# Kernel tuning notes

Measured on AMD Instinct MI355X. Metric: run time of the kernel, lower is better.

## Reference

```python
import jax, jax.numpy as jnp
import numpy as np

DIM = 1024
NUM_HEADS = 16
HEAD_DIM = DIM // NUM_HEADS
SCALE = 1.0 / np.sqrt(HEAD_DIM)
B, S = 2, 2048


def setup_inputs() -> dict:
    key = jax.random.key(0)
    ks = jax.random.split(key, 10)
    std = 1.0 / np.sqrt(DIM)
    return {
        "x": jax.random.normal(ks[0], (B, S, DIM), dtype=jnp.float32),
        "Wq": jax.random.normal(ks[1], (DIM, DIM), dtype=jnp.float32) * std,
        "bq": jnp.zeros((DIM,), dtype=jnp.float32),
        "Wk": jax.random.normal(ks[2], (DIM, DIM), dtype=jnp.float32) * std,
        "bk": jnp.zeros((DIM,), dtype=jnp.float32),
        "Wv": jax.random.normal(ks[3], (DIM, DIM), dtype=jnp.float32) * std,
        "bv": jnp.zeros((DIM,), dtype=jnp.float32),
        "Wo": jax.random.normal(ks[4], (DIM, DIM), dtype=jnp.float32) * std,
        "bo": jnp.zeros((DIM,), dtype=jnp.float32),
        "mobius_weight": jax.random.normal(ks[5], (1,), dtype=jnp.float32) * 0.01,
    }


def _split_heads(t):
    b, s, _ = t.shape
    return t.reshape(b, s, NUM_HEADS, HEAD_DIM).transpose(0, 2, 1, 3)  # bhsd


def reference(x, Wq, bq, Wk, bk, Wv, bv, Wo, bo, mobius_weight):
    q = _split_heads(x @ Wq.T + bq)
    k = _split_heads(x @ Wk.T + bk)
    v = _split_heads(x @ Wv.T + bv)

    # similarity: plain QK^T
    similarity = jnp.einsum('bhqd,bhkd->bhqk', q, k)
    # mobius cross-term: q_omega . k_pi + q_pi . k_omega
    h = HEAD_DIM // 2
    q_om, q_pi = q[..., :h], q[..., h:]
    k_om, k_pi = k[..., :h], k[..., h:]
    mobius = jnp.einsum('bhqd,bhkd->bhqk', q_om, k_pi) + \
             jnp.einsum('bhqd,bhkd->bhqk', q_pi, k_om)

    incidence = (similarity + mobius_weight[0] * mobius) * SCALE
    attn = jax.nn.softmax(incidence, axis=-1)
    out = jnp.einsum('bhqk,bhkd->bhqd', attn, v)
    out = out.transpose(0, 2, 1, 3).reshape(x.shape[0], x.shape[1], DIM)
    return out @ Wo.T + bo
```

## Files before the change

### kernel.cpp

```cpp
#include <hip/hip_runtime.h>


typedef __attribute__((ext_vector_type(8))) short short8;
typedef __attribute__((ext_vector_type(4))) short s16x4;
typedef __attribute__((ext_vector_type(4))) float f32x4;
typedef __attribute__((ext_vector_type(16))) float f32x16;
typedef __attribute__((ext_vector_type(8))) __bf16 bf16x8;
typedef __attribute__((ext_vector_type(4))) unsigned uint4v;

__device__ __forceinline__ float exp2fa(float x) {
  return __builtin_amdgcn_exp2f(x);
}
__device__ __forceinline__ short f2bf(float f) {
  unsigned u = __builtin_bit_cast(unsigned, f);
  u = u + 0x7fffu + ((u >> 16) & 1u);
  return (short)(u >> 16);
}
__device__ __forceinline__ f32x4 mfma16(bf16x8 a, bf16x8 b, f32x4 c) {
  return __builtin_amdgcn_mfma_f32_16x16x32_bf16(a, b, c, 0, 0, 0);
}
__device__ __forceinline__ f32x16 mfma32(bf16x8 a, bf16x8 b, f32x16 c) {
  return __builtin_amdgcn_mfma_f32_32x32x16_bf16(a, b, c, 0, 0, 0);
}
__device__ __forceinline__ void gload_lds16(const void* g, void* l) {
  __builtin_amdgcn_global_load_lds(
      (const __attribute__((address_space(1))) unsigned int*)g,
      (__attribute__((address_space(3))) unsigned int*)l, 16, 0, 0);
}
__device__ __forceinline__ unsigned pkbf(float a, float b) {
  unsigned r;
  asm("v_cvt_pk_bf16_f32 %0, %1, %2" : "=v"(r) : "v"(a), "v"(b));
  return r;
}
__device__ __forceinline__ void plswap(unsigned& a, unsigned& b) {
  asm volatile("v_permlane32_swap_b32 %0, %1" : "+v"(a), "+v"(b));
}
__device__ __forceinline__ bf16x8 pack8(float x0, float x1, float x2, float x3,
                                        float x4, float x5, float x6, float x7) {
  unsigned a0 = pkbf(x0, x1), a1 = pkbf(x2, x3);
  unsigned a2 = pkbf(x4, x5), a3 = pkbf(x6, x7);
  plswap(a0, a2);
  plswap(a1, a3);
  uint4v u = {a0, a1, a2, a3};
  return __builtin_bit_cast(bf16x8, u);
}

__global__ void cast_all_kernel(const float* x, const float* w0, const float* w1,
                                const float* w2, const float* w3, short* xo,
                                short* o0, short* o1, short* o2, short* o3) {
  const float* in; short* out;
  const int r = blockIdx.y;
  size_t off;
  if (r < 4) { in = x; out = xo; off = (size_t)r * 131072; }
  else {
    switch (r) {
      case 4: in = w0; out = o0; break;
      case 5: in = w1; out = o1; break;
      case 6: in = w2; out = o2; break;
      default: in = w3; out = o3; break;
    }
    off = 0;
  }
  const size_t i = off + blockIdx.x * 256 + threadIdx.x;
  const float4* p = (const float4*)in;
  float4 a = p[2 * i], b = p[2 * i + 1];
  short8 o;
  o[0] = f2bf(a.x); o[1] = f2bf(a.y); o[2] = f2bf(a.z); o[3] = f2bf(a.w);
  o[4] = f2bf(b.x); o[5] = f2bf(b.y); o[6] = f2bf(b.z); o[7] = f2bf(b.w);
  ((short8*)out)[i] = o;
}

constexpr int GK = 1024, GN = 1024;
constexpr float QSCALE = 0.125f * 1.44269504088896340736f;

template <int EP>
__device__ __forceinline__ void gemm_body(char* lds, const short* __restrict__ A,
                                          const short* __restrict__ W,
                                          const float* __restrict__ bias,
                                          void* __restrict__ C,
                                          const float* __restrict__ mwp) {
  const int tid = threadIdx.x;
  const int l = tid & 63, w = tid >> 6;
  const int wr = w >> 2, wc = w & 3;
  const int ncb = (wc >> 1) * 64 + (wc & 1) * 16;
  const int m0 = blockIdx.y * 128, n0 = blockIdx.x * 128;

  f32x4 acc[4][2] = {};

  const int srow = tid >> 3, sc8 = tid & 7, wv = tid >> 6;
  for (int kb = 0; kb < GK / 64; ++kb) {
    const int k0 = kb * 64;
#pragma unroll
    for (int p = 0; p < 2; ++p) {
      const int ra = p * 64 + srow;
      gload_lds16(A + (size_t)(m0 + ra) * GK + k0 + ((sc8 ^ (ra & 7)) * 8),
                  lds + p * 8192 + wv * 1024);
      gload_lds16(W + (size_t)(n0 + ra) * GK + k0 + ((sc8 ^ (ra & 7)) * 8),
                  lds + 16384 + p * 8192 + wv * 1024);
    }
    __syncthreads();
#pragma unroll
    for (int ks = 0; ks < 2; ++ks) {
      bf16x8 af[4], bfr[2];
      const int chunk = ks * 4 + (l >> 4);
#pragma unroll
      for (int mf = 0; mf < 4; ++mf) {
        const int mt = wr * 64 + mf * 16 + (l & 15);
        af[mf] = *(const bf16x8*)(lds + mt * 128 + ((chunk ^ (mt & 7)) * 16));
      }
#pragma unroll
      for (int nf = 0; nf < 2; ++nf) {
        const int nt = ncb + nf * 32 + (l & 15);
        bfr[nf] = *(const bf16x8*)(lds + 16384 + nt * 128 + ((chunk ^ (nt & 7)) * 16));
      }
#pragma unroll
      for (int mf = 0; mf < 4; ++mf)
#pragma unroll
        for (int nf = 0; nf < 2; ++nf)
          acc[mf][nf] = mfma16(af[mf], bfr[nf], acc[mf][nf]);
    }
    __syncthreads();
  }

  const float mwv = (EP == 1) ? mwp[0] : 0.f;
#pragma unroll
  for (int mf = 0; mf < 4; ++mf)
#pragma unroll
    for (int nf = 0; nf < 2; ++nf) {
      const int n = n0 + ncb + nf * 32 + (l & 15);
      const int mb = m0 + wr * 64 + mf * 16 + (l >> 4) * 4;
      if (EP == 1) {
        const float bv = bias[n], bv2 = bias[n ^ 32];
        const int h = n >> 6, c = (n >> 3) & 7, j = n & 7;
#pragma unroll
        for (int r = 0; r < 4; ++r) {
          const int m = mb + r;
          const int b = m >> 11, s = m & 2047;
          const float v =
              acc[mf][nf][r] + bv + mwv * (acc[mf][nf ^ 1][r] + bv2);
          ((short*)C)[(size_t)(b * 16 + h) * 131072 + (s >> 5) * 2048 + c * 256 +
                      (s & 31) * 8 + j] = f2bf(v);
        }
      } else if (EP == 2) {
        const int h = n >> 6, w2 = (n >> 5) & 1, dlo = n & 31;
        s16x4 v;
#pragma unroll
        for (int r = 0; r < 4; ++r) v[r] = f2bf(acc[mf][nf][r] + bias[n]);
        const int b = mb >> 11, s = mb & 2047;
        *(s16x4*)((short*)C + (size_t)(b * 16 + h) * 131072 + (s >> 6) * 4096 +
                  w2 * 2048 + ((s >> 3) & 7) * 256 + dlo * 8 + (s & 7)) = v;
      } else {
        const float bv = bias[n];
#pragma unroll
        for (int r = 0; r < 4; ++r) {
          const int m = mb + r;
          float v = acc[mf][nf][r] + bv;
          if (EP == 0) v *= QSCALE;
          if (EP == 3)
            ((float*)C)[(size_t)m * GN + n] = v;
          else
            ((short*)C)[(size_t)m * GN + n] = f2bf(v);
        }
      }
    }
}

__global__ __launch_bounds__(512, 4) void gemm_qkv_kernel(
    const short* __restrict__ A, const short* Wq, const short* Wk, const short* Wv,
    const float* bq, const float* bk, const float* bv, short* q, short* kf,
    short* vf, const float* mw) {
  __shared__ __align__(16) char lds[32768];
  if (blockIdx.z == 0) gemm_body<0>(lds, A, Wq, bq, q, nullptr);
  else if (blockIdx.z == 1) gemm_body<1>(lds, A, Wk, bk, kf, mw);
  else gemm_body<2>(lds, A, Wv, bv, vf, nullptr);
}

__global__ __launch_bounds__(512, 4) void gemm_out_kernel(const short* __restrict__ A,
                                                          const short* __restrict__ W,
                                                          const float* __restrict__ bias,
                                                          float* __restrict__ C) {
  __shared__ __align__(16) char lds[32768];
  gemm_body<3>(lds, A, W, bias, C, nullptr);
}

__global__ __launch_bounds__(256, 3) void attn_kernel(const short* __restrict__ Q,
                                                      const short* __restrict__ Kf,
                                                      const short* __restrict__ Vf,
                                                      short* __restrict__ O) {
  constexpr int S = 2048;
  constexpr int NT = S / 128;
  __shared__ float mbuf[2][32][64];
  __shared__ float lbuf[64];
  const int tid = threadIdx.x;
  const int l = tid & 63, w = tid >> 6;
  const int lo = l & 31, hi = l >> 5;
  const int wq = w & 1, par = w >> 1;
  const int bid = blockIdx.x;
  const int sub = bid >> 3;
  const int x = sub & 31;
  const int y = (bid & 7) * 4 + (sub >> 5);
  const int b = y >> 4, h = y & 15;
  const int q0 = x * 64 + wq * 32;
  const size_t base = (size_t)b * S * 1024 + h * 64;
  const size_t fbase = (size_t)y * 131072;

  bf16x8 qf[4];
  {
    const short* qp = Q + base + (size_t)(q0 + lo) * 1024 + hi * 8;
#pragma unroll
    for (int ds = 0; ds < 4; ++ds) qf[ds] = *(const bf16x8*)(qp + ds * 16);
  }

  const int voff = hi * 256 + lo * 8;
  const short* kp = Kf + fbase + par * 4096 + voff;
  const short* vp = Vf + fbase + par * 4096 + voff;

  bf16x8 kf[8], vf[8];
#pragma unroll
  for (int ds = 0; ds < 4; ++ds) {
    kf[ds]     = *(const bf16x8*)(kp + ds * 512);
    kf[4 + ds] = *(const bf16x8*)(kp + 2048 + ds * 512);
    vf[ds]     = *(const bf16x8*)(vp + ds * 512);
    vf[4 + ds] = *(const bf16x8*)(vp + 2048 + ds * 512);
  }

  f32x16 o0 = {}, o1 = {};
  float lrow = 0.f;

  f32x16 st0 = {}, st1 = {};
  __builtin_amdgcn_s_setprio(1);
#pragma unroll
  for (int ds = 0; ds < 4; ++ds) {
    st0 = mfma32(kf[ds], qf[ds], st0);
    st1 = mfma32(kf[4 + ds], qf[ds], st1);
  }
  __builtin_amdgcn_s_setprio(0);
  kp += 8192;
#pragma unroll
  for (int ds = 0; ds < 4; ++ds) {
    kf[ds]     = *(const bf16x8*)(kp + ds * 512);
    kf[4 + ds] = *(const bf16x8*)(kp + 2048 + ds * 512);
  }

  for (int i = 0; i < NT - 1; ++i) {
#pragma unroll
    for (int r = 0; r < 16; ++r) st0[r] = exp2fa(st0[r]);
#pragma unroll
    for (int r = 0; r < 16; ++r) st1[r] = exp2fa(st1[r]);
    float ts[8];
#pragma unroll
    for (int r = 0; r < 8; ++r)
      ts[r] = (st0[r] + st0[r + 8]) + (st1[r] + st1[r + 8]);
#pragma unroll
    for (int d = 4; d >= 1; d >>= 1)
#pragma unroll
      for (int r = 0; r < 4; ++r)
        if (r < d) ts[r] += ts[r + d];
    lrow += ts[0];

    bf16x8 pf[4];
    pf[0] = pack8(st0[0], st0[1], st0[2], st0[3], st0[4], st0[5], st0[6], st0[7]);
    pf[1] = pack8(st0[8], st0[9], st0[10], st0[11], st0[12], st0[13], st0[14], st0[15]);
    pf[2] = pack8(st1[0], st1[1], st1[2], st1[3], st1[4], st1[5], st1[6], st1[7]);
    pf[3] = pack8(st1[8], st1[9], st1[10], st1[11], st1[12], st1[13], st1[14], st1[15]);

    __builtin_amdgcn_s_setprio(1);
#pragma unroll
    for (int r = 0; r < 16; ++r) { st0[r] = 0.f; st1[r] = 0.f; }
#pragma unroll
    for (int ds = 0; ds < 4; ++ds) {
      st0 = mfma32(kf[ds], qf[ds], st0);
      st1 = mfma32(kf[4 + ds], qf[ds], st1);
    }
#pragma unroll
    for (int kv = 0; kv < 4; ++kv) {
      o0 = mfma32(vf[kv], pf[kv], o0);
      o1 = mfma32(vf[4 + kv], pf[kv], o1);
    }
    __builtin_amdgcn_s_setprio(0);

    kp += 8192;
    vp += 8192;
#pragma unroll
    for (int ds = 0; ds < 4; ++ds) {
      kf[ds]     = *(const bf16x8*)(kp + ds * 512);
      kf[4 + ds] = *(const bf16x8*)(kp + 2048 + ds * 512);
      vf[ds]     = *(const bf16x8*)(vp + ds * 512);
      vf[4 + ds] = *(const bf16x8*)(vp + 2048 + ds * 512);
    }
  }

  {
#pragma unroll
    for (int r = 0; r < 16; ++r) st0[r] = exp2fa(st0[r]);
#pragma unroll
    for (int r = 0; r < 16; ++r) st1[r] = exp2fa(st1[r]);
    float ts[8];
#pragma unroll
    for (int r = 0; r < 8; ++r)
      ts[r] = (st0[r] + st0[r + 8]) + (st1[r] + st1[r + 8]);
#pragma unroll
    for (int d = 4; d >= 1; d >>= 1)
#pragma unroll
      for (int r = 0; r < 4; ++r)
        if (r < d) ts[r] += ts[r + d];
    lrow += ts[0];

    bf16x8 pf[4];
    pf[0] = pack8(st0[0], st0[1], st0[2], st0[3], st0[4], st0[5], st0[6], st0[7]);
    pf[1] = pack8(st0[8], st0[9], st0[10], st0[11], st0[12], st0[13], st0[14], st0[15]);
    pf[2] = pack8(st1[0], st1[1], st1[2], st1[3], st1[4], st1[5], st1[6], st1[7]);
    pf[3] = pack8(st1[8], st1[9], st1[10], st1[11], st1[12], st1[13], st1[14], st1[15]);
    __builtin_amdgcn_s_setprio(1);
#pragma unroll
    for (int kv = 0; kv < 4; ++kv) {
      o0 = mfma32(vf[kv], pf[kv], o0);
      o1 = mfma32(vf[4 + kv], pf[kv], o1);
    }
    __builtin_amdgcn_s_setprio(0);
  }

  lrow += __shfl_xor(lrow, 32);

  if (par == 1) {
#pragma unroll
    for (int g = 0; g < 4; ++g) {
      const int c0 = (2 * g + hi) ^ (lo & 15);
      const int c1 = (8 + 2 * g + hi) ^ (lo & 15);
      f32x4 v0, v1;
#pragma unroll
      for (int r = 0; r < 4; ++r) { v0[r] = o0[g * 4 + r]; v1[r] = o1[g * 4 + r]; }
      *(f32x4*)(&mbuf[wq][lo][c0 * 4]) = v0;
      *(f32x4*)(&mbuf[wq][lo][c1 * 4]) = v1;
    }
    if (hi == 0) lbuf[wq * 32 + lo] = lrow;
  }
  __syncthreads();
  if (par == 0) {
#pragma unroll
    for (int g = 0; g < 4; ++g) {
      const int c0 = (2 * g + hi) ^ (lo & 15);
      const int c1 = (8 + 2 * g + hi) ^ (lo & 15);
      f32x4 v0 = *(const f32x4*)(&mbuf[wq][lo][c0 * 4]);
      f32x4 v1 = *(const f32x4*)(&mbuf[wq][lo][c1 * 4]);
#pragma unroll
      for (int r = 0; r < 4; ++r) { o0[g * 4 + r] += v0[r]; o1[g * 4 + r] += v1[r]; }
    }
    const float inv = 1.0f / (lrow + lbuf[wq * 32 + lo]);
    short* Op = O + base + (size_t)(q0 + lo) * 1024;
#pragma unroll
    for (int g = 0; g < 4; ++g) {
      s16x4 v0, v1;
#pragma unroll
      for (int r = 0; r < 4; ++r) {
        v0[r] = f2bf(o0[g * 4 + r] * inv);
        v1[r] = f2bf(o1[g * 4 + r] * inv);
      }
      *(s16x4*)(Op + 8 * g + 4 * hi) = v0;
      *(s16x4*)(Op + 32 + 8 * g + 4 * hi) = v1;
    }
  }
}

extern "C" void kernel_launch(void* const* d_in, const int* in_sizes, int n_in,
                              void* d_out, int out_size, void* d_ws, size_t ws_size,
                              hipStream_t stream) {
  const float* x  = (const float*)d_in[0];
  const float* Wq = (const float*)d_in[1];
  const float* bq = (const float*)d_in[2];
  const float* Wk = (const float*)d_in[3];
  const float* bk = (const float*)d_in[4];
  const float* Wv = (const float*)d_in[5];
  const float* bv = (const float*)d_in[6];
  const float* Wo = (const float*)d_in[7];
  const float* bo = (const float*)d_in[8];
  const float* mw = (const float*)d_in[9];
  float* out = (float*)d_out;
  char* ws = (char*)d_ws;
  const size_t MB = (size_t)1 << 20;

  short* xb  = (short*)(ws + 0 * MB);
  short* wqb = (short*)(ws + 8 * MB);
  short* wkb = (short*)(ws + 10 * MB);
  short* wvb = (short*)(ws + 12 * MB);
  short* wob = (short*)(ws + 14 * MB);
  short* qb  = (short*)(ws + 16 * MB);
  short* kfb = (short*)(ws + 24 * MB);
  short* vfb = (short*)(ws + 32 * MB);
  short* ob  = (short*)(ws + 40 * MB);

  cast_all_kernel<<<dim3(512, 8), 256, 0, stream>>>(x, Wq, Wk, Wv, Wo, xb, wqb,
                                                    wkb, wvb, wob);
  gemm_qkv_kernel<<<dim3(8, 32, 3), 512, 0, stream>>>(xb, wqb, wkb, wvb, bq, bk, bv,
                                                      qb, kfb, vfb, mw);
  attn_kernel<<<1024, 256, 0, stream>>>(qb, kfb, vfb, ob);
  gemm_out_kernel<<<dim3(8, 32), 512, 0, stream>>>(ob, wob, bo, out);
}
```

Baseline: 118.7 us.

## Give output projection its own 64x128-tile GEMM kernel with doubled grid

Replaces the shared gemm_body path for the output projection with a dedicated kernel that uses 64x128 tiles, a smaller LDS footprint and a grid twice as tall, so more blocks fill the GPU for the 4096x1024 GEMM. It also lowers the attention kernel's launch-bounds occupancy hint from 3 to 2 blocks per CU, which gives the compiler more registers per thread. The new GEMM is single-buffered, syncs twice per k-step and has 2x2 fragments per wave, so it may be latency bound. The smaller tiles also reuse each loaded operand less.

```diff
diff --git a/kernel.cpp b/kernel.cpp
--- a/kernel.cpp
+++ b/kernel.cpp
@@ -156,10 +156,7 @@
           const int m = mb + r;
           float v = acc[mf][nf][r] + bv;
           if (EP == 0) v *= QSCALE;
-          if (EP == 3)
-            ((float*)C)[(size_t)m * GN + n] = v;
-          else
-            ((short*)C)[(size_t)m * GN + n] = f2bf(v);
+          ((short*)C)[(size_t)m * GN + n] = f2bf(v);
         }
       }
     }
@@ -179,11 +176,64 @@
                                                           const short* __restrict__ W,
                                                           const float* __restrict__ bias,
                                                           float* __restrict__ C) {
-  __shared__ __align__(16) char lds[32768];
-  gemm_body<3>(lds, A, W, bias, C, nullptr);
-}
-
-__global__ __launch_bounds__(256, 3) void attn_kernel(const short* __restrict__ Q,
+  __shared__ __align__(16) char lds[24576];
+  const int tid = threadIdx.x;
+  const int l = tid & 63, w = tid >> 6;
+  const int wr = w >> 2, wc = w & 3;
+  const int m0 = blockIdx.y * 64, n0 = blockIdx.x * 128;
+
+  f32x4 acc[2][2] = {};
+
+  const int srow = tid >> 3, sc8 = tid & 7, wv = tid >> 6;
+  const int sra = srow & 63;
+  for (int kb = 0; kb < GK / 64; ++kb) {
+    const int k0 = kb * 64;
+    gload_lds16(A + (size_t)(m0 + sra) * GK + k0 + ((sc8 ^ (sra & 7)) * 8),
+                lds + wv * 1024);
+#pragma unroll
+    for (int p = 0; p < 2; ++p) {
+      const int rw = p * 64 + srow;
+      gload_lds16(W + (size_t)(n0 + rw) * GK + k0 + ((sc8 ^ (rw & 7)) * 8),
+                  lds + 8192 + p * 8192 + wv * 1024);
+    }
+    __syncthreads();
+#pragma unroll
+    for (int ks = 0; ks < 2; ++ks) {
+      bf16x8 af[2], bfr[2];
+      const int chunk = ks * 4 + (l >> 4);
+#pragma unroll
+      for (int mf = 0; mf < 2; ++mf) {
+        const int mt = wr * 32 + mf * 16 + (l & 15);
+        af[mf] = *(const bf16x8*)(lds + mt * 128 + ((chunk ^ (mt & 7)) * 16));
+      }
+#pragma unroll
+      for (int nf = 0; nf < 2; ++nf) {
+        const int nt = wc * 32 + nf * 16 + (l & 15);
+        bfr[nf] = *(const bf16x8*)(lds + 8192 + nt * 128 + ((chunk ^ (nt & 7)) * 16));
+      }
+#pragma unroll
+      for (int mf = 0; mf < 2; ++mf)
+#pragma unroll
+        for (int nf = 0; nf < 2; ++nf)
+          acc[mf][nf] = mfma16(af[mf], bfr[nf], acc[mf][nf]);
+    }
+    __syncthreads();
+  }
+
+#pragma unroll
+  for (int mf = 0; mf < 2; ++mf)
+#pragma unroll
+    for (int nf = 0; nf < 2; ++nf) {
+      const int n = n0 + wc * 32 + nf * 16 + (l & 15);
+      const int mb = m0 + wr * 32 + mf * 16 + (l >> 4) * 4;
+      const float bv = bias[n];
+#pragma unroll
+      for (int r = 0; r < 4; ++r)
+        C[(size_t)(mb + r) * GN + n] = acc[mf][nf][r] + bv;
+    }
+}
+
+__global__ __launch_bounds__(256, 2) void attn_kernel(const short* __restrict__ Q,
                                                       const short* __restrict__ Kf,
                                                       const short* __restrict__ Vf,
                                                       short* __restrict__ O) {
@@ -394,5 +444,5 @@
   gemm_qkv_kernel<<<dim3(8, 32, 3), 512, 0, stream>>>(xb, wqb, wkb, wvb, bq, bk, bv,
                                                       qb, kfb, vfb, mw);
   attn_kernel<<<1024, 256, 0, stream>>>(qb, kfb, vfb, ob);
-  gemm_out_kernel<<<dim3(8, 32), 512, 0, stream>>>(ob, wob, bo, out);
-}
+  gemm_out_kernel<<<dim3(8, 64), 512, 0, stream>>>(ob, wob, bo, out);
+}
```

Measured after the change: 117.4 us. Within noise of the previous version (-1.2%).
